# Kernel optimization log

Hardware: AMD Instinct MI355X
Metric: run time of the kernel (lower is better)

Reference implementation:

```python
import jax, jax.numpy as jnp
import numpy as np

L, B, S, H, V = 6, 8, 2048, 768, 32000
FF = 4 * H
EPS = 1e-5


def _ln(x, g, b):
    m = x.mean(-1, keepdims=True)
    v = ((x - m) ** 2).mean(-1, keepdims=True)
    return (x - m) / jnp.sqrt(v + EPS) * g + b


def setup_inputs() -> dict:
    key = jax.random.key(0)
    ks = iter(jax.random.split(key, 32))
    std = 0.02
    n = lambda shape: jax.random.normal(next(ks), shape, dtype=jnp.float32) * std
    inp = {
        'input_ids': jax.random.randint(next(ks), (B, S), 0, V, dtype=jnp.int64),
        'attention_mask': jnp.ones((B, S), dtype=jnp.int32),
        'tok_emb': n((V, H)),
        'pos_emb': n((S, H)),
        'Wq': n((L, H, H)), 'bq': n((L, H)),
        'Wk': n((L, H, H)), 'bk': n((L, H)),
        'Wv': n((L, H, H)), 'bv': n((L, H)),
        'Wo': n((L, H, H)), 'bo': n((L, H)),
        'ln1_g': jnp.ones((L, H), jnp.float32), 'ln1_b': jnp.zeros((L, H), jnp.float32),
        'ln2_g': jnp.ones((L, H), jnp.float32), 'ln2_b': jnp.zeros((L, H), jnp.float32),
        'W1': n((L, H, FF)), 'b1': n((L, FF)),
        'W2': n((L, FF, H)), 'b2': n((L, H)),
        'fln_g': jnp.ones((H,), jnp.float32), 'fln_b': jnp.zeros((H,), jnp.float32),
        'cls_W': n((H, 1)), 'cls_b': n((1,)),
    }
    return inp


def reference(input_ids, attention_mask, tok_emb, pos_emb, Wq, bq, Wk, bk, Wv, bv,
              Wo, bo, ln1_g, ln1_b, ln2_g, ln2_b, W1, b1, W2, b2,
              fln_g, fln_b, cls_W, cls_b):
    x = tok_emb[input_ids] + pos_emb[None, :S, :]  # [B,S,H]
    causal = jnp.triu(jnp.ones((S, S), dtype=bool), 1)  # True above diagonal
    pad = ~(attention_mask.astype(bool))[:, None, :]    # [B,1,S] True where padded
    full_mask = causal[None, :, :] | pad                # [B,S,S]
    scale = 1.0 / (H ** 0.5)
    for i in range(L):
        # --- attention block (pre-LN) ---
        h = _ln(x, ln1_g[i], ln1_b[i])
        q = h @ Wq[i] + bq[i]
        k = h @ Wk[i] + bk[i]
        v = h @ Wv[i] + bv[i]
        scores = jnp.einsum('bqd,bkd->bqk', q, k) * scale
        scores = jnp.where(full_mask, -jnp.inf, scores)
        attn = jax.nn.softmax(scores, axis=-1)
        o = jnp.einsum('bqk,bkd->bqd', attn, v) @ Wo[i] + bo[i]
        x = o + x
        # --- FFN block ---
        h = _ln(x, ln2_g[i], ln2_b[i])
        x = jax.nn.gelu(h @ W1[i] + b1[i], approximate=False) @ W2[i] + b2[i] + x
    x = _ln(x, fln_g, fln_b)
    # select hidden state of last non-padded token per row
    m = attention_mask.astype(jnp.int32)
    last = m.sum(1) - 1                      # [B]
    x_last = x[jnp.arange(B), last]          # [B,H]
    logits = x_last @ cls_W + cls_b          # [B,1]
    return logits
```

## Files before the change

### kernel.cpp

```cpp
#include <hip/hip_runtime.h>
#include <hip/hip_bf16.h>

#define Bn 8
#define Sn 2048
#define Hn 768
#define FFn 3072
#define Ln 6
#define BSn (Bn * Sn)
#define CQ 512
#define LN_EPS 1e-5f

typedef __hip_bfloat16 bf16;
typedef __bf16 bf16x8 __attribute__((ext_vector_type(8)));
typedef float f32x4 __attribute__((ext_vector_type(4)));

__device__ __forceinline__ float b2f(bf16 v) { return __bfloat162float(v); }
__device__ __forceinline__ void stc(float* p, float v) { *p = v; }
__device__ __forceinline__ void stc(bf16* p, float v) { *p = __float2bfloat16(v); }

union Pk8 { float4 v; bf16 h[8]; };

__device__ __forceinline__ void gld16(const bf16* g, short* l) {
  __builtin_amdgcn_global_load_lds(
      (const __attribute__((address_space(1))) unsigned int*)g,
      (__attribute__((address_space(3))) unsigned int*)l, 16, 0, 0);
}

#define BAR() __builtin_amdgcn_s_barrier()
#define LGKM0()                                            \
  {                                                        \
    asm volatile("s_waitcnt lgkmcnt(0)" ::: "memory");     \
    __builtin_amdgcn_sched_barrier(0);                     \
  }
#define VMC(n) asm volatile("s_waitcnt vmcnt(" #n ")" ::: "memory")

__global__ void __launch_bounds__(256) embed_kernel(
    const int* __restrict__ ids, const float* __restrict__ tok,
    const float* __restrict__ pos, float* __restrict__ x) {
  long t = blockIdx.x;
  int s = (int)(t & (Sn - 1));
  long id = ids[t];
  const float* tr = tok + id * Hn;
  const float* pr = pos + (long)s * Hn;
  float* xr = x + t * Hn;
  for (int d = threadIdx.x; d < Hn; d += 256)
    xr[d] = tr[d] + pr[d];
}

__global__ void __launch_bounds__(256) transpose_all_kernel(
    const float* __restrict__ Wq_l, const float* __restrict__ Wk_l,
    const float* __restrict__ Wv_l, const float* __restrict__ Wo_l,
    const float* __restrict__ W1_l, const float* __restrict__ W2_l,
    bf16* __restrict__ wt) {
  int id = blockIdx.x;
  const float* W;
  bf16* Wt;
  int K, N, tile, tilesX;
  if (id < 2304) {
    int w = id / 576;
    tile = id - w * 576;
    W = (w == 0) ? Wq_l : (w == 1) ? Wk_l : (w == 2) ? Wv_l : Wo_l;
    Wt = wt + (size_t)w * Hn * Hn;
    K = Hn; N = Hn; tilesX = Hn / 32;
  } else if (id < 4608) {
    tile = id - 2304;
    W = W1_l;
    Wt = wt + 4 * (size_t)Hn * Hn;
    K = Hn; N = FFn; tilesX = FFn / 32;
  } else {
    tile = id - 4608;
    W = W2_l;
    Wt = wt + 4 * (size_t)Hn * Hn + (size_t)Hn * FFn;
    K = FFn; N = Hn; tilesX = Hn / 32;
  }
  int n0 = (tile % tilesX) * 32, k0 = (tile / tilesX) * 32;

  __shared__ float t[32][33];
  int tx = threadIdx.x & 31, ty = threadIdx.x >> 5;
#pragma unroll
  for (int i = 0; i < 32; i += 8)
    t[ty + i][tx] = W[(long)(k0 + ty + i) * N + n0 + tx];
  __syncthreads();
#pragma unroll
  for (int i = 0; i < 32; i += 8)
    stc(Wt + (long)(n0 + ty + i) * K + k0 + tx, t[tx][ty + i]);
}

__global__ void __launch_bounds__(256) ln_kernel(
    const float* __restrict__ x, const float* __restrict__ g,
    const float* __restrict__ b, bf16* __restrict__ out) {
  long token = blockIdx.x;
  const float* xr = x + token * Hn;
  bf16* orow = out + token * Hn;
  int tid = threadIdx.x;

  float vals[3];
  float s1 = 0.f;
#pragma unroll
  for (int i = 0; i < 3; i++) {
    vals[i] = xr[tid + 256 * i];
    s1 += vals[i];
  }
  __shared__ float sb[4];
  __shared__ float stat[2];
#pragma unroll
  for (int off = 32; off > 0; off >>= 1) s1 += __shfl_down(s1, off, 64);
  if ((tid & 63) == 0) sb[tid >> 6] = s1;
  __syncthreads();
  if (tid == 0) stat[0] = (sb[0] + sb[1] + sb[2] + sb[3]) * (1.0f / Hn);
  __syncthreads();
  float mean = stat[0];

  float s2 = 0.f;
#pragma unroll
  for (int i = 0; i < 3; i++) {
    float d = vals[i] - mean;
    s2 += d * d;
  }
#pragma unroll
  for (int off = 32; off > 0; off >>= 1) s2 += __shfl_down(s2, off, 64);
  if ((tid & 63) == 0) sb[tid >> 6] = s2;
  __syncthreads();
  if (tid == 0)
    stat[1] = rsqrtf((sb[0] + sb[1] + sb[2] + sb[3]) * (1.0f / Hn) + LN_EPS);
  __syncthreads();
  float inv = stat[1];

#pragma unroll
  for (int i = 0; i < 3; i++) {
    int d = tid + 256 * i;
    stc(orow + d, (vals[i] - mean) * inv * g[d] + b[d]);
  }
}

template <int EPI, typename CT>
__global__ void __launch_bounds__(512) gemm256_kernel(
    const bf16* __restrict__ A, const bf16* __restrict__ Bt,
    const float* __restrict__ bias, const float* __restrict__ res,
    CT* __restrict__ C, int M, int N, int K,
    const float* __restrict__ bias2, const float* __restrict__ bias3) {
  __shared__ short lds[65536];
  int tid = threadIdx.x;
  int wave = tid >> 6, lane = tid & 63;
  int wm = wave >> 2, wn = wave & 3;
  int quad = lane >> 4, l16 = lane & 15;
  int swz = (l16 & 7) << 4;
  int g = lane >> 3;
  int kswz = ((lane & 7) ^ g) * 8;

  int nwg = gridDim.x, orig = blockIdx.x;
  int q8 = nwg >> 3, r8 = nwg & 7;
  int xcd = orig & 7, loc = orig >> 3;
  int wg = (xcd < r8 ? xcd * (q8 + 1) : r8 * (q8 + 1) + (xcd - r8) * q8) + loc;
  int gx = N >> 8;
  long colBase = (long)(wg % gx) * 256;
  long rowBase = (long)(wg / gx) * 256;

  const bf16* Ag = A + rowBase * K;
  const bf16* Bg = Bt + colBase * K;

  f32x4 acc[8][4] = {};
  bf16x8 af[4][2], bfr[2][2][2];

#define STAGEA(T, odd)                                                     \
  {                                                                        \
    short* base_ = lds + ((T) & 1) * 32768;                                \
    long kt_ = (long)(T) * 64;                                             \
    _Pragma("unroll") for (int j_ = 0; j_ < 2; j_++) {                     \
      int c_ = wave * 2 + j_;                                              \
      int r0_ = (odd) * 64 + ((c_ >> 3) << 7) + ((c_ & 7) << 3);           \
      gld16(Ag + (long)(r0_ + g) * K + kt_ + kswz, base_ + r0_ * 64);      \
    }                                                                      \
  }
#define STAGEB(T, odd)                                                     \
  {                                                                        \
    short* base_ = lds + ((T) & 1) * 32768 + 16384;                        \
    long kt_ = (long)(T) * 64;                                             \
    _Pragma("unroll") for (int j_ = 0; j_ < 2; j_++) {                     \
      int c_ = wave * 2 + j_;                                              \
      int r0_ = (odd) * 32 + ((c_ >> 2) << 6) + ((c_ & 3) << 3);           \
      gld16(Bg + (long)(r0_ + g) * K + kt_ + kswz, base_ + r0_ * 64);      \
    }                                                                      \
  }
#define LOADA(T, h)                                                        \
  {                                                                        \
    const char* base_ = (const char*)(lds + ((T) & 1) * 32768);            \
    _Pragma("unroll") for (int i_ = 0; i_ < 4; i_++) {                     \
      const char* rp_ = base_ + (wm * 128 + (h) * 64 + i_ * 16 + l16) * 128; \
      _Pragma("unroll") for (int s_ = 0; s_ < 2; s_++)                     \
          af[i_][s_] = *(const bf16x8*)(rp_ + ((s_ * 64 + quad * 16) ^ swz)); \
    }                                                                      \
  }
#define LOADB(T, nh)                                                       \
  {                                                                        \
    const char* base_ = (const char*)(lds + ((T) & 1) * 32768 + 16384);    \
    _Pragma("unroll") for (int j_ = 0; j_ < 2; j_++) {                     \
      const char* rp_ = base_ + (wn * 64 + (nh) * 32 + j_ * 16 + l16) * 128; \
      _Pragma("unroll") for (int s_ = 0; s_ < 2; s_++)                     \
          bfr[nh][j_][s_] = *(const bf16x8*)(rp_ + ((s_ * 64 + quad * 16) ^ swz)); \
    }                                                                      \
  }
#define MFMA_PH(h, nh)                                                     \
  __builtin_amdgcn_s_setprio(1);                                           \
  _Pragma("unroll") for (int i_ = 0; i_ < 4; i_++)                         \
      _Pragma("unroll") for (int j_ = 0; j_ < 2; j_++)                     \
          _Pragma("unroll") for (int s_ = 0; s_ < 2; s_++)                 \
              acc[(h) * 4 + i_][(nh) * 2 + j_] =                           \
                  __builtin_amdgcn_mfma_f32_16x16x32_bf16(                 \
                      af[i_][s_], bfr[nh][j_][s_],                         \
                      acc[(h) * 4 + i_][(nh) * 2 + j_], 0, 0, 0);          \
  __builtin_amdgcn_s_setprio(0);

  int NT = K >> 6;
  STAGEA(0, 0); STAGEB(0, 0); STAGEB(0, 1); STAGEA(0, 1);
  STAGEA(1, 0); STAGEB(1, 0); STAGEB(1, 1);
  VMC(6);
  BAR();

  for (int T = 0; T < NT; T++) {
    LOADA(T, 0); LOADB(T, 0);
    if (T + 1 < NT) STAGEA(T + 1, 1);
    BAR(); LGKM0(); MFMA_PH(0, 0); BAR();
    LOADB(T, 1);
    if (T + 2 < NT) STAGEA(T + 2, 0);
    BAR(); LGKM0(); MFMA_PH(0, 1); BAR();
    LOADA(T, 1);
    if (T + 2 < NT) STAGEB(T + 2, 0);
    BAR(); LGKM0(); MFMA_PH(1, 1); BAR();
    if (T + 2 < NT) { STAGEB(T + 2, 1); VMC(6); }
    else { VMC(0); }
    BAR(); MFMA_PH(1, 0); BAR();
  }

#pragma unroll
  for (int mi = 0; mi < 8; mi++) {
#pragma unroll
    for (int nj = 0; nj < 4; nj++) {
      int col = (int)colBase + wn * 64 + nj * 16 + l16;
      long row0 = rowBase + wm * 128 + mi * 16 + quad * 4;
      if (EPI == 4) {
        if (col < 1536) {
          float bv = col < 768 ? bias[col] : bias2[col - 768];
          bf16* dst = (bf16*)C + (col < 768 ? 0 : (size_t)BSn * Hn - Hn);
#pragma unroll
          for (int r = 0; r < 4; r++)
            stc(dst + (row0 + r) * Hn + col, acc[mi][nj][r] + bv);
        } else {
          int vcol = col - 1536;
          float bv = bias3[vcol];
          union { uint2 w; bf16 h[4]; } pk;
          long bb = row0 >> 11;
          long s = row0 & (Sn - 1);
#pragma unroll
          for (int r = 0; r < 4; r++)
            pk.h[r] = __float2bfloat16(acc[mi][nj][r] + bv);
          bf16* vT = (bf16*)C + 2 * (size_t)BSn * Hn;
          *reinterpret_cast<uint2*>(vT + (bb * Hn + vcol) * Sn + s) = pk.w;
        }
      } else {
        float bv = bias[col];
#pragma unroll
        for (int r = 0; r < 4; r++) {
          long row = row0 + r;
          float v = acc[mi][nj][r] + bv;
          if (EPI == 1) v += res[row * N + col];
          if (EPI == 2) v = 0.5f * v * (1.0f + erff(v * 0.70710678118654752f));
          stc(C + row * N + col, v);
        }
      }
    }
  }
#undef STAGEA
#undef STAGEB
#undef LOADA
#undef LOADB
#undef MFMA_PH
}

__global__ void __launch_bounds__(256) qk_mfma_kernel(
    const bf16* __restrict__ q, const bf16* __restrict__ k,
    bf16* __restrict__ sc, int q0) {
  int kBase = blockIdx.x * 128;
  int qBase = q0 + blockIdx.y * 128;
  if (kBase > qBase + 127) return;
  int b = blockIdx.z;
  const bf16* Ag = q + ((long)b * Sn + qBase) * Hn;
  const bf16* Bg = k + ((long)b * Sn + kBase) * Hn;

  __shared__ short As[128 * 32];
  __shared__ short Bs[128 * 32];
  int tid = threadIdx.x;
  int wave = tid >> 6, lane = tid & 63;
  int waveM = wave >> 1, waveN = wave & 1;
  int quad = lane >> 4, l16 = lane & 15;
  int srow = lane >> 2;
  int schunk = (lane & 3) * 8;

  f32x4 acc[4][4] = {};

  for (int kt = 0; kt < Hn; kt += 32) {
#pragma unroll
    for (int c = 0; c < 2; c++) {
      int r0 = wave * 32 + c * 16;
      gld16(Ag + (long)(r0 + srow) * Hn + kt + schunk, &As[r0 * 32]);
      gld16(Bg + (long)(r0 + srow) * Hn + kt + schunk, &Bs[r0 * 32]);
    }
    __syncthreads();

    bf16x8 af[4], bfrg[4];
#pragma unroll
    for (int t = 0; t < 4; t++)
      af[t] = *(const bf16x8*)&As[(waveM * 64 + t * 16 + l16) * 32 + quad * 8];
#pragma unroll
    for (int u = 0; u < 4; u++)
      bfrg[u] = *(const bf16x8*)&Bs[(waveN * 64 + u * 16 + l16) * 32 + quad * 8];
#pragma unroll
    for (int t = 0; t < 4; t++)
#pragma unroll
      for (int u = 0; u < 4; u++)
        acc[t][u] = __builtin_amdgcn_mfma_f32_16x16x32_bf16(af[t], bfrg[u],
                                                            acc[t][u], 0, 0, 0);
    __syncthreads();
  }

  const float scale = 0.03608439182435161f;
#pragma unroll
  for (int t = 0; t < 4; t++)
#pragma unroll
    for (int u = 0; u < 4; u++) {
      int col = kBase + waveN * 64 + u * 16 + l16;
#pragma unroll
      for (int r = 0; r < 4; r++) {
        long qRel = (long)(qBase - q0) + waveM * 64 + t * 16 + quad * 4 + r;
        stc(sc + ((long)b * CQ + qRel) * Sn + col, acc[t][u][r] * scale);
      }
    }
}

__global__ void __launch_bounds__(256) pv_mfma_kernel(
    const bf16* __restrict__ p, const bf16* __restrict__ vT,
    bf16* __restrict__ o, int q0) {
  int colBase = blockIdx.x * 128;
  int qBase = q0 + blockIdx.y * 128;
  int b = blockIdx.z;
  int klimit = qBase + 128;
  const bf16* Ag = p + ((long)b * CQ + (qBase - q0)) * Sn;
  const bf16* Bg = vT + ((long)b * Hn + colBase) * Sn;

  __shared__ short As[128 * 32];
  __shared__ short Bs[128 * 32];
  int tid = threadIdx.x;
  int wave = tid >> 6, lane = tid & 63;
  int waveM = wave >> 1, waveN = wave & 1;
  int quad = lane >> 4, l16 = lane & 15;
  int srow = lane >> 2;
  int schunk = (lane & 3) * 8;

  f32x4 acc[4][4] = {};

  for (int kt = 0; kt < klimit; kt += 32) {
#pragma unroll
    for (int c = 0; c < 2; c++) {
      int r0 = wave * 32 + c * 16;
      gld16(Ag + (long)(r0 + srow) * Sn + kt + schunk, &As[r0 * 32]);
      gld16(Bg + (long)(r0 + srow) * Sn + kt + schunk, &Bs[r0 * 32]);
    }
    __syncthreads();

    bf16x8 af[4], bfrg[4];
#pragma unroll
    for (int t = 0; t < 4; t++)
      af[t] = *(const bf16x8*)&As[(waveM * 64 + t * 16 + l16) * 32 + quad * 8];
#pragma unroll
    for (int u = 0; u < 4; u++)
      bfrg[u] = *(const bf16x8*)&Bs[(waveN * 64 + u * 16 + l16) * 32 + quad * 8];
#pragma unroll
    for (int t = 0; t < 4; t++)
#pragma unroll
      for (int u = 0; u < 4; u++)
        acc[t][u] = __builtin_amdgcn_mfma_f32_16x16x32_bf16(af[t], bfrg[u],
                                                            acc[t][u], 0, 0, 0);
    __syncthreads();
  }

#pragma unroll
  for (int t = 0; t < 4; t++)
#pragma unroll
    for (int u = 0; u < 4; u++) {
      int col = colBase + waveN * 64 + u * 16 + l16;
#pragma unroll
      for (int r = 0; r < 4; r++) {
        long qAbs = (long)qBase + waveM * 64 + t * 16 + quad * 4 + r;
        stc(o + ((long)b * Sn + qAbs) * Hn + col, acc[t][u][r]);
      }
    }
}

__global__ void __launch_bounds__(256) softmax_kernel(
    bf16* __restrict__ sc, const int* __restrict__ mask, int q0) {
  int qRel = blockIdx.x;
  int b = blockIdx.y;
  int qg = q0 + qRel;
  bf16* row = sc + ((long)b * CQ + qRel) * Sn;
  const int* mrow = mask + b * Sn;
  int tid = threadIdx.x;
  int n = qg + 1;
  int limit = (qg & ~127) + 128;
  int k0 = tid * 8;

  Pk8 pk;
  pk.v = *reinterpret_cast<const float4*>(row + k0);
  int4 m0 = *reinterpret_cast<const int4*>(mrow + k0);
  int4 m1 = *reinterpret_cast<const int4*>(mrow + k0 + 4);
  int mm[8] = {m0.x, m0.y, m0.z, m0.w, m1.x, m1.y, m1.z, m1.w};

  float sv[8];
  float lmax = -1e30f;
#pragma unroll
  for (int j = 0; j < 8; j++) {
    int kk = k0 + j;
    float s = (kk < n && mm[j] != 0) ? b2f(pk.h[j]) : -1e30f;
    sv[j] = s;
    lmax = fmaxf(lmax, s);
  }
  __shared__ float sb[4];
  __shared__ float stat;
#pragma unroll
  for (int off = 32; off > 0; off >>= 1)
    lmax = fmaxf(lmax, __shfl_down(lmax, off, 64));
  if ((tid & 63) == 0) sb[tid >> 6] = lmax;
  __syncthreads();
  if (tid == 0) stat = fmaxf(fmaxf(sb[0], sb[1]), fmaxf(sb[2], sb[3]));
  __syncthreads();
  float gmax = stat;

  float ev[8];
  float lsum = 0.f;
#pragma unroll
  for (int j = 0; j < 8; j++) {
    float e = (sv[j] > -1e29f) ? __expf(sv[j] - gmax) : 0.f;
    ev[j] = e;
    lsum += e;
  }
#pragma unroll
  for (int off = 32; off > 0; off >>= 1) lsum += __shfl_down(lsum, off, 64);
  if ((tid & 63) == 0) sb[tid >> 6] = lsum;
  __syncthreads();
  if (tid == 0) stat = sb[0] + sb[1] + sb[2] + sb[3];
  __syncthreads();
  float inv = 1.0f / stat;

  if (k0 < limit) {
    Pk8 o;
#pragma unroll
    for (int j = 0; j < 8; j++)
      o.h[j] = __float2bfloat16((k0 + j < n) ? ev[j] * inv : 0.f);
    *reinterpret_cast<float4*>(row + k0) = o.v;
  }
}

__global__ void __launch_bounds__(256) cls_kernel(
    const bf16* __restrict__ h, const int* __restrict__ mask,
    const float* __restrict__ clsW, const float* __restrict__ clsb,
    float* __restrict__ out) {
  int b = blockIdx.x;
  int tid = threadIdx.x;
  __shared__ float sb[4];
  __shared__ int ib[4];
  __shared__ int lastsh;

  int ls = 0;
  for (int s = tid; s < Sn; s += 256) ls += mask[b * Sn + s];
#pragma unroll
  for (int off = 32; off > 0; off >>= 1) ls += __shfl_down(ls, off, 64);
  if ((tid & 63) == 0) ib[tid >> 6] = ls;
  __syncthreads();
  if (tid == 0) lastsh = ib[0] + ib[1] + ib[2] + ib[3] - 1;
  __syncthreads();
  int last = lastsh;

  const bf16* row = h + ((long)b * Sn + last) * Hn;
  float acc = 0.f;
  for (int d = tid; d < Hn; d += 256) acc += b2f(row[d]) * clsW[d];
#pragma unroll
  for (int off = 32; off > 0; off >>= 1) acc += __shfl_down(acc, off, 64);
  if ((tid & 63) == 0) sb[tid >> 6] = acc;
  __syncthreads();
  if (tid == 0) out[b] = sb[0] + sb[1] + sb[2] + sb[3] + clsb[0];
}

extern "C" void kernel_launch(void* const* d_in, const int* in_sizes, int n_in,
                              void* d_out, int out_size, void* d_ws,
                              size_t ws_size, hipStream_t stream) {
  const int* ids     = (const int*)d_in[0];
  const int* mask    = (const int*)d_in[1];
  const float* tok   = (const float*)d_in[2];
  const float* pos   = (const float*)d_in[3];
  const float* Wq    = (const float*)d_in[4];
  const float* bq    = (const float*)d_in[5];
  const float* Wk    = (const float*)d_in[6];
  const float* bk    = (const float*)d_in[7];
  const float* Wv    = (const float*)d_in[8];
  const float* bv    = (const float*)d_in[9];
  const float* Wo    = (const float*)d_in[10];
  const float* bo    = (const float*)d_in[11];
  const float* ln1g  = (const float*)d_in[12];
  const float* ln1b  = (const float*)d_in[13];
  const float* ln2g  = (const float*)d_in[14];
  const float* ln2b  = (const float*)d_in[15];
  const float* W1    = (const float*)d_in[16];
  const float* b1    = (const float*)d_in[17];
  const float* W2    = (const float*)d_in[18];
  const float* b2    = (const float*)d_in[19];
  const float* flng  = (const float*)d_in[20];
  const float* flnb  = (const float*)d_in[21];
  const float* clsW  = (const float*)d_in[22];
  const float* clsb  = (const float*)d_in[23];

  float* x = (float*)d_ws;
  bf16* h  = (bf16*)(x + (size_t)BSn * Hn);
  bf16* cb = h + (size_t)BSn * Hn;
  bf16* qb = cb;
  bf16* kb = cb + (size_t)BSn * Hn;
  bf16* vtb = cb + 2 * (size_t)BSn * Hn;
  bf16* scb = cb + 3 * (size_t)BSn * Hn;
  bf16* wt = cb + (size_t)BSn * FFn;
  bf16* wqT = wt;
  bf16* woT = wqT + 3 * (size_t)Hn * Hn;
  bf16* w1T = woT + (size_t)Hn * Hn;
  bf16* w2T = w1T + (size_t)Hn * FFn;

  const int M = BSn;
  dim3 blk(256);
  dim3 blk512(512);
  dim3 gridQK(Sn / 128, CQ / 128, Bn);
  dim3 gridSM(CQ, Bn);
  dim3 gridPV(Hn / 128, CQ / 128, Bn);

  embed_kernel<<<BSn, blk, 0, stream>>>(ids, tok, pos, x);

  for (int l = 0; l < Ln; l++) {
    const float* Wq_l = Wq + (size_t)l * Hn * Hn;
    const float* Wk_l = Wk + (size_t)l * Hn * Hn;
    const float* Wv_l = Wv + (size_t)l * Hn * Hn;
    const float* Wo_l = Wo + (size_t)l * Hn * Hn;
    const float* W1_l = W1 + (size_t)l * Hn * FFn;
    const float* W2_l = W2 + (size_t)l * FFn * Hn;

    transpose_all_kernel<<<6912, blk, 0, stream>>>(Wq_l, Wk_l, Wv_l, Wo_l,
                                                   W1_l, W2_l, wt);

    ln_kernel<<<BSn, blk, 0, stream>>>(x, ln1g + l * Hn, ln1b + l * Hn, h);
    gemm256_kernel<4, bf16><<<576, blk512, 0, stream>>>(
        h, wqT, bq + l * Hn, nullptr, qb, M, 3 * Hn, Hn,
        bk + l * Hn, bv + l * Hn);
    for (int c = 0; c < Sn / CQ; c++) {
      int q0 = c * CQ;
      qk_mfma_kernel<<<gridQK, blk, 0, stream>>>(qb, kb, scb, q0);
      softmax_kernel<<<gridSM, blk, 0, stream>>>(scb, mask, q0);
      pv_mfma_kernel<<<gridPV, blk, 0, stream>>>(scb, vtb, h, q0);
    }
    gemm256_kernel<1, float><<<192, blk512, 0, stream>>>(
        h, woT, bo + l * Hn, x, x, M, Hn, Hn, nullptr, nullptr);

    ln_kernel<<<BSn, blk, 0, stream>>>(x, ln2g + l * Hn, ln2b + l * Hn, h);
    gemm256_kernel<2, bf16><<<768, blk512, 0, stream>>>(
        h, w1T, b1 + l * FFn, nullptr, cb, M, FFn, Hn, nullptr, nullptr);
    gemm256_kernel<1, float><<<192, blk512, 0, stream>>>(
        cb, w2T, b2 + l * Hn, x, x, M, Hn, FFn, nullptr, nullptr);
  }

  ln_kernel<<<BSn, blk, 0, stream>>>(x, flng, flnb, h);
  cls_kernel<<<Bn, blk, 0, stream>>>(h, mask, clsW, clsb, (float*)d_out);
}
```

Before: 4.001 ms.

## Unroll GEMM main loop by two with precomputed addresses and faster GELU

The GEMM k-loop is unrolled into pairs of tiles, so the double-buffer indices become compile-time constants. Global and LDS addresses are computed once before the loop and advanced by pointer increments, which removes per-iteration index arithmetic and the tail branches inside the loop. The last two tiles are handled by an explicit epilogue. Separately, erff in the GELU epilogue is replaced by the Abramowitz-Stegun polynomial approximation with __expf, which cuts epilogue ALU cost but adds roughly 1e-7 absolute error in erf. The pair unroll assumes an even tile count, which holds for K=768 and K=3072.

```diff
diff --git a/kernel.cpp b/kernel.cpp
--- a/kernel.cpp
+++ b/kernel.cpp
@@ -33,6 +33,18 @@
     __builtin_amdgcn_sched_barrier(0);                     \
   }
 #define VMC(n) asm volatile("s_waitcnt vmcnt(" #n ")" ::: "memory")
+
+__device__ __forceinline__ float gelu_exact(float v) {
+  float a = fabsf(v) * 0.70710678118654752f;
+  float t = 1.0f / (1.0f + 0.3275911f * a);
+  float poly = t * (0.254829592f +
+               t * (-0.284496736f +
+               t * (1.421413741f +
+               t * (-1.453152027f + t * 1.061405429f))));
+  float er = 1.0f - poly * __expf(-a * a);
+  er = v < 0.f ? -er : er;
+  return 0.5f * v * (1.0f + er);
+}
 
 __global__ void __launch_bounds__(256) embed_kernel(
     const int* __restrict__ ids, const float* __restrict__ tok,
@@ -156,81 +168,114 @@
   long colBase = (long)(wg % gx) * 256;
   long rowBase = (long)(wg / gx) * 256;
 
-  const bf16* Ag = A + rowBase * K;
-  const bf16* Bg = Bt + colBase * K;
+  const bf16* aSrc = A + rowBase * K + (long)g * K + kswz;
+  const bf16* bSrc = Bt + colBase * K + (long)g * K + kswz;
+
+  int r0A[2][2], r0B[2][2], sA[2][2], sB[2][2];
+#pragma unroll
+  for (int o = 0; o < 2; o++)
+#pragma unroll
+    for (int j = 0; j < 2; j++) {
+      int c = wave * 2 + j;
+      r0A[o][j] = o * 64 + ((c >> 3) << 7) + ((c & 7) << 3);
+      r0B[o][j] = o * 32 + ((c >> 2) << 6) + ((c & 3) << 3);
+      sA[o][j] = r0A[o][j] * K;
+      sB[o][j] = r0B[o][j] * K;
+    }
+
+  char* lb = (char*)lds;
+  const char* aRd0 = lb + (wm * 128 + l16) * 128 + ((quad * 16) ^ swz);
+  const char* aRd1 = lb + (wm * 128 + l16) * 128 + ((64 + quad * 16) ^ swz);
+  const char* bRd0 = lb + 65536 + (wn * 64 + l16) * 128 + ((quad * 16) ^ swz);
+  const char* bRd1 = lb + 65536 + (wn * 64 + l16) * 128 + ((64 + quad * 16) ^ swz);
 
   f32x4 acc[8][4] = {};
   bf16x8 af[4][2], bfr[2][2][2];
 
-#define STAGEA(T, odd)                                                     \
-  {                                                                        \
-    short* base_ = lds + ((T) & 1) * 32768;                                \
-    long kt_ = (long)(T) * 64;                                             \
-    _Pragma("unroll") for (int j_ = 0; j_ < 2; j_++) {                     \
-      int c_ = wave * 2 + j_;                                              \
-      int r0_ = (odd) * 64 + ((c_ >> 3) << 7) + ((c_ & 7) << 3);           \
-      gld16(Ag + (long)(r0_ + g) * K + kt_ + kswz, base_ + r0_ * 64);      \
-    }                                                                      \
-  }
-#define STAGEB(T, odd)                                                     \
-  {                                                                        \
-    short* base_ = lds + ((T) & 1) * 32768 + 16384;                        \
-    long kt_ = (long)(T) * 64;                                             \
-    _Pragma("unroll") for (int j_ = 0; j_ < 2; j_++) {                     \
-      int c_ = wave * 2 + j_;                                              \
-      int r0_ = (odd) * 32 + ((c_ >> 2) << 6) + ((c_ & 3) << 3);           \
-      gld16(Bg + (long)(r0_ + g) * K + kt_ + kswz, base_ + r0_ * 64);      \
-    }                                                                      \
-  }
-#define LOADA(T, h)                                                        \
-  {                                                                        \
-    const char* base_ = (const char*)(lds + ((T) & 1) * 32768);            \
-    _Pragma("unroll") for (int i_ = 0; i_ < 4; i_++) {                     \
-      const char* rp_ = base_ + (wm * 128 + (h) * 64 + i_ * 16 + l16) * 128; \
-      _Pragma("unroll") for (int s_ = 0; s_ < 2; s_++)                     \
-          af[i_][s_] = *(const bf16x8*)(rp_ + ((s_ * 64 + quad * 16) ^ swz)); \
-    }                                                                      \
-  }
-#define LOADB(T, nh)                                                       \
-  {                                                                        \
-    const char* base_ = (const char*)(lds + ((T) & 1) * 32768 + 16384);    \
-    _Pragma("unroll") for (int j_ = 0; j_ < 2; j_++) {                     \
-      const char* rp_ = base_ + (wn * 64 + (nh) * 32 + j_ * 16 + l16) * 128; \
-      _Pragma("unroll") for (int s_ = 0; s_ < 2; s_++)                     \
-          bfr[nh][j_][s_] = *(const bf16x8*)(rp_ + ((s_ * 64 + quad * 16) ^ swz)); \
-    }                                                                      \
-  }
-#define MFMA_PH(h, nh)                                                     \
-  __builtin_amdgcn_s_setprio(1);                                           \
-  _Pragma("unroll") for (int i_ = 0; i_ < 4; i_++)                         \
-      _Pragma("unroll") for (int j_ = 0; j_ < 2; j_++)                     \
-          _Pragma("unroll") for (int s_ = 0; s_ < 2; s_++)                 \
-              acc[(h) * 4 + i_][(nh) * 2 + j_] =                           \
-                  __builtin_amdgcn_mfma_f32_16x16x32_bf16(                 \
-                      af[i_][s_], bfr[nh][j_][s_],                         \
-                      acc[(h) * 4 + i_][(nh) * 2 + j_], 0, 0, 0);          \
+#define STAGEA(ODD, BUF, KOFF)                                              \
+  {                                                                         \
+    gld16(aSrc + sA[ODD][0] + (KOFF),                                       \
+          (short*)(lb + (BUF) * 32768 + r0A[ODD][0] * 128));                \
+    gld16(aSrc + sA[ODD][1] + (KOFF),                                       \
+          (short*)(lb + (BUF) * 32768 + r0A[ODD][1] * 128));                \
+  }
+#define STAGEB(ODD, BUF, KOFF)                                              \
+  {                                                                         \
+    gld16(bSrc + sB[ODD][0] + (KOFF),                                       \
+          (short*)(lb + 65536 + (BUF) * 32768 + r0B[ODD][0] * 128));        \
+    gld16(bSrc + sB[ODD][1] + (KOFF),                                       \
+          (short*)(lb + 65536 + (BUF) * 32768 + r0B[ODD][1] * 128));        \
+  }
+#define LOADA(BUF, H)                                                       \
+  {                                                                         \
+    _Pragma("unroll") for (int i_ = 0; i_ < 4; i_++) {                      \
+      af[i_][0] = *(const bf16x8*)(aRd0 + (BUF) * 32768 +                   \
+                                   ((H) * 64 + i_ * 16) * 128);             \
+      af[i_][1] = *(const bf16x8*)(aRd1 + (BUF) * 32768 +                   \
+                                   ((H) * 64 + i_ * 16) * 128);             \
+    }                                                                       \
+  }
+#define LOADB(BUF, NH)                                                      \
+  {                                                                         \
+    _Pragma("unroll") for (int j_ = 0; j_ < 2; j_++) {                      \
+      bfr[NH][j_][0] = *(const bf16x8*)(bRd0 + (BUF) * 32768 +              \
+                                        ((NH) * 32 + j_ * 16) * 128);       \
+      bfr[NH][j_][1] = *(const bf16x8*)(bRd1 + (BUF) * 32768 +              \
+                                        ((NH) * 32 + j_ * 16) * 128);       \
+    }                                                                       \
+  }
+#define MFMA_PH(h, nh)                                                      \
+  __builtin_amdgcn_s_setprio(1);                                            \
+  _Pragma("unroll") for (int i_ = 0; i_ < 4; i_++)                          \
+      _Pragma("unroll") for (int j_ = 0; j_ < 2; j_++)                      \
+          _Pragma("unroll") for (int s_ = 0; s_ < 2; s_++)                  \
+              acc[(h) * 4 + i_][(nh) * 2 + j_] =                            \
+                  __builtin_amdgcn_mfma_f32_16x16x32_bf16(                  \
+                      af[i_][s_], bfr[nh][j_][s_],                          \
+                      acc[(h) * 4 + i_][(nh) * 2 + j_], 0, 0, 0);           \
   __builtin_amdgcn_s_setprio(0);
 
   int NT = K >> 6;
-  STAGEA(0, 0); STAGEB(0, 0); STAGEB(0, 1); STAGEA(0, 1);
-  STAGEA(1, 0); STAGEB(1, 0); STAGEB(1, 1);
+  STAGEA(0, 0, 0); STAGEB(0, 0, 0); STAGEB(1, 0, 0); STAGEA(1, 0, 0);
+  STAGEA(0, 1, 64); STAGEB(0, 1, 64); STAGEB(1, 1, 64);
   VMC(6);
   BAR();
 
-  for (int T = 0; T < NT; T++) {
-    LOADA(T, 0); LOADB(T, 0);
-    if (T + 1 < NT) STAGEA(T + 1, 1);
+  int pairs = (NT - 2) >> 1;
+  for (int p = 0; p < pairs; p++) {
+    LOADA(0, 0); LOADB(0, 0); STAGEA(1, 1, 64);
     BAR(); LGKM0(); MFMA_PH(0, 0); BAR();
-    LOADB(T, 1);
-    if (T + 2 < NT) STAGEA(T + 2, 0);
+    LOADB(0, 1); STAGEA(0, 0, 128);
     BAR(); LGKM0(); MFMA_PH(0, 1); BAR();
-    LOADA(T, 1);
-    if (T + 2 < NT) STAGEB(T + 2, 0);
+    LOADA(0, 1); STAGEB(0, 0, 128);
     BAR(); LGKM0(); MFMA_PH(1, 1); BAR();
-    if (T + 2 < NT) { STAGEB(T + 2, 1); VMC(6); }
-    else { VMC(0); }
+    STAGEB(1, 0, 128); VMC(6);
     BAR(); MFMA_PH(1, 0); BAR();
-  }
+    LOADA(1, 0); LOADB(1, 0); STAGEA(1, 0, 128);
+    BAR(); LGKM0(); MFMA_PH(0, 0); BAR();
+    LOADB(1, 1); STAGEA(0, 1, 192);
+    BAR(); LGKM0(); MFMA_PH(0, 1); BAR();
+    LOADA(1, 1); STAGEB(0, 1, 192);
+    BAR(); LGKM0(); MFMA_PH(1, 1); BAR();
+    STAGEB(1, 1, 192); VMC(6);
+    BAR(); MFMA_PH(1, 0); BAR();
+    aSrc += 128; bSrc += 128;
+  }
+  LOADA(0, 0); LOADB(0, 0); STAGEA(1, 1, 64);
+  BAR(); LGKM0(); MFMA_PH(0, 0); BAR();
+  LOADB(0, 1);
+  BAR(); LGKM0(); MFMA_PH(0, 1); BAR();
+  LOADA(0, 1);
+  BAR(); LGKM0(); MFMA_PH(1, 1); BAR();
+  VMC(0);
+  BAR(); MFMA_PH(1, 0); BAR();
+  LOADA(1, 0); LOADB(1, 0);
+  BAR(); LGKM0(); MFMA_PH(0, 0); BAR();
+  LOADB(1, 1);
+  BAR(); LGKM0(); MFMA_PH(0, 1); BAR();
+  LOADA(1, 1);
+  BAR(); LGKM0(); MFMA_PH(1, 1); BAR();
+  BAR(); MFMA_PH(1, 0); BAR();
 
 #pragma unroll
   for (int mi = 0; mi < 8; mi++) {
@@ -264,7 +309,7 @@
           long row = row0 + r;
           float v = acc[mi][nj][r] + bv;
           if (EPI == 1) v += res[row * N + col];
-          if (EPI == 2) v = 0.5f * v * (1.0f + erff(v * 0.70710678118654752f));
+          if (EPI == 2) v = gelu_exact(v);
           stc(C + row * N + col, v);
         }
       }
```

Measured after the change: 3.925 ms. No clear change (-1.9%).
